# Optimization experiments

Measured on AMD Instinct MI355X. Metric: run time of the kernel, lower is better.

Reference implementation:

```python
import jax, jax.numpy as jnp
import numpy as np

N, IN_C, HID, OUT = 100000, 128, 128, 64
E, EP = 500000, 100000


def _glorot(key, shape):
    fan_in, fan_out = shape[0], shape[1]
    s = jnp.sqrt(6.0 / (fan_in + fan_out))
    return jax.random.uniform(key, shape, jnp.float32, -s, s)


def setup_inputs() -> dict:
    key = jax.random.key(0)
    ks = jax.random.split(key, 10)
    x = jax.random.normal(ks[0], (N, IN_C), jnp.float32)
    edge_index = jax.random.randint(ks[1], (2, E), 0, N, jnp.int64)
    pos_edge_index = jax.random.randint(ks[2], (2, EP), 0, N, jnp.int64)
    neg_edge_index = jax.random.randint(ks[3], (2, EP), 0, N, jnp.int64)
    return {
        "x": x,
        "edge_index": edge_index,
        "pos_edge_index": pos_edge_index,
        "neg_edge_index": neg_edge_index,
        "Wl1": _glorot(ks[4], (IN_C, HID)),
        "Wr1": _glorot(ks[5], (IN_C, HID)),
        "b1": jnp.zeros((HID,), jnp.float32),
        "Wl2": _glorot(ks[6], (HID, OUT)),
        "Wr2": _glorot(ks[7], (HID, OUT)),
        "b2": jnp.zeros((OUT,), jnp.float32),
    }


def sage_conv(x, src, dst, Wl, Wr, b):
    # mean aggregation of neighbor features: messages x[src] scattered to dst
    agg = jax.ops.segment_sum(x[src], dst, num_segments=N)  # (N, D)
    deg = jax.ops.segment_sum(jnp.ones((src.shape[0],), x.dtype), dst, num_segments=N)
    mean = agg / jnp.clip(deg, 1.0, None)[:, None]
    return mean @ Wl + x @ Wr + b


def decode_dot(z, ei):
    return (z[ei[0]] * z[ei[1]]).sum(axis=1)  # (E,)


def reference(x, edge_index, pos_edge_index, neg_edge_index, Wl1, Wr1, b1, Wl2, Wr2, b2):
    src, dst = edge_index[0], edge_index[1]
    h = jax.nn.relu(sage_conv(x, src, dst, Wl1, Wr1, b1))  # dropout off (eval)
    z = sage_conv(h, src, dst, Wl2, Wr2, b2)
    return decode_dot(z, pos_edge_index), decode_dot(z, neg_edge_index)
```

## Files before the change

### kernel.cpp

```cpp
#include <hip/hip_runtime.h>

#define N_NODES 100000
#define NE 500000
#define NEP 100000
#define NBLK_SCAN ((N_NODES + 255) / 256)

typedef short bf16x8 __attribute__((ext_vector_type(8)));
typedef float f32x4  __attribute__((ext_vector_type(4)));
typedef ushort ushort8v __attribute__((ext_vector_type(8)));

__device__ inline ushort f2bf(float f) {
    uint u = __builtin_bit_cast(uint, f);
    return (ushort)((u + 0x7FFFu + ((u >> 16) & 1u)) >> 16);
}
__device__ inline float bf2f(ushort h) {
    uint u = ((uint)h) << 16;
    return __builtin_bit_cast(float, u);
}
__device__ inline float bflo(uint v) { return __builtin_bit_cast(float, v << 16); }
__device__ inline float bfhi(uint v) { return __builtin_bit_cast(float, v & 0xFFFF0000u); }

__global__ __launch_bounds__(256) void hist_kernel(
    const int* __restrict__ ei, int* __restrict__ cnt) {
    int e = blockIdx.x * 256 + threadIdx.x;
    if (e >= NE) return;
    atomicAdd(&cnt[ei[NE + e]], 1);
}

__global__ __launch_bounds__(256) void scan1_kernel(
    const int* __restrict__ cnt, int* __restrict__ off, int* __restrict__ sums) {
    __shared__ int buf[256];
    int t = threadIdx.x;
    int i = blockIdx.x * 256 + t;
    int v = (i < N_NODES) ? cnt[i] : 0;
    buf[t] = v;
    __syncthreads();
#pragma unroll
    for (int d = 1; d < 256; d <<= 1) {
        int add = (t >= d) ? buf[t - d] : 0;
        __syncthreads();
        buf[t] += add;
        __syncthreads();
    }
    if (i < N_NODES) off[i] = buf[t] - v;
    if (t == 255) sums[blockIdx.x] = buf[255];
}

__global__ __launch_bounds__(256) void scan23_kernel(
    int* __restrict__ off, int* __restrict__ off2, const int* __restrict__ sums) {
    __shared__ int red[256];
    int bid = blockIdx.x, t = threadIdx.x;
    int v = 0;
    if (t < bid) v += sums[t];
    if (t + 256 < bid) v += sums[t + 256];
    red[t] = v;
    __syncthreads();
#pragma unroll
    for (int d = 128; d > 0; d >>= 1) {
        if (t < d) red[t] += red[t + d];
        __syncthreads();
    }
    int pre = red[0];
    int i = bid * 256 + t;
    if (i < N_NODES) {
        int o = off[i] + pre;
        off[i] = o;
        off2[i] = o;
    }
    if (i == 0) off[N_NODES] = NE;
}

__global__ __launch_bounds__(256) void fill_kernel(
    const int* __restrict__ ei, int* __restrict__ off2, int* __restrict__ srcS) {
    int e = blockIdx.x * 256 + threadIdx.x;
    if (e >= NE) return;
    int src = ei[e];
    int dst = ei[NE + e];
    int pos = atomicAdd(&off2[dst], 1);
    srcS[pos] = src;
}

__global__ __launch_bounds__(256) void prep_kernel(
    const float* __restrict__ x, ushort* __restrict__ xb,
    const float* __restrict__ Wl1, const float* __restrict__ Wr1,
    ushort* __restrict__ b1h,
    const float* __restrict__ Wl2, const float* __restrict__ Wr2,
    ushort* __restrict__ b2h, int* __restrict__ cnt) {
    int b = blockIdx.x;
    if (b < 6250) {
        size_t i = ((size_t)b * 256 + threadIdx.x) * 8;
        float4 v0 = *reinterpret_cast<const float4*>(x + i);
        float4 v1 = *reinterpret_cast<const float4*>(x + i + 4);
        ushort8v o;
        o[0] = f2bf(v0.x); o[1] = f2bf(v0.y); o[2] = f2bf(v0.z); o[3] = f2bf(v0.w);
        o[4] = f2bf(v1.x); o[5] = f2bf(v1.y); o[6] = f2bf(v1.z); o[7] = f2bf(v1.w);
        *reinterpret_cast<ushort8v*>(xb + i) = o;
    } else if (b < 6250 + 128) {
        int gid = (b - 6250) * 256 + threadIdx.x;
        int r = gid & 7, lane = (gid >> 3) & 63, t = (gid >> 9) & 7, ks = gid >> 12;
        int k = ks * 32 + ((lane >> 4) << 3) + r;
        int n = t * 16 + (lane & 15);
        float v = (k < 128) ? Wl1[k * 128 + n] : Wr1[(k - 128) * 128 + n];
        b1h[gid] = f2bf(v);
    } else if (b < 6442) {
        int gid = (b - 6378) * 256 + threadIdx.x;
        int r = gid & 7, lane = (gid >> 3) & 63, t = (gid >> 9) & 7, ks = gid >> 12;
        int k = ks * 32 + ((lane >> 4) << 3) + r;
        int col = t * 16 + (lane & 15);
        float v = (col < 64) ? Wl2[k * 64 + col] : Wr2[k * 64 + (col - 64)];
        b2h[gid] = f2bf(v);
    } else {
        int i = ((b - 6442) * 256 + threadIdx.x) * 4;
        *reinterpret_cast<int4*>(cnt + i) = make_int4(0, 0, 0, 0);
    }
}

__global__ __launch_bounds__(256) void agg_mean_kernel(
    const ushort* __restrict__ xb, const int* __restrict__ off,
    const int* __restrict__ srcS, ushort* __restrict__ meanH) {
    int n = blockIdx.x * 16 + (threadIdx.x >> 4);
    int l = threadIdx.x & 15;
    int s0 = off[n], s1 = off[n + 1];
    float a0 = 0.f, a1 = 0.f, a2 = 0.f, a3 = 0.f;
    float a4 = 0.f, a5 = 0.f, a6 = 0.f, a7 = 0.f;
    int k = s0;
#define ACCM(v)                                                   \
    { a0 += bflo((v).x); a1 += bfhi((v).x);                       \
      a2 += bflo((v).y); a3 += bfhi((v).y);                       \
      a4 += bflo((v).z); a5 += bfhi((v).z);                       \
      a6 += bflo((v).w); a7 += bfhi((v).w); }
    for (; k + 4 <= s1; k += 4) {
        int sa = srcS[k], sb = srcS[k + 1], sc = srcS[k + 2], sd = srcS[k + 3];
        uint4 va = *(const uint4*)(xb + (size_t)sa * 128 + l * 8);
        uint4 vb = *(const uint4*)(xb + (size_t)sb * 128 + l * 8);
        uint4 vc = *(const uint4*)(xb + (size_t)sc * 128 + l * 8);
        uint4 vd = *(const uint4*)(xb + (size_t)sd * 128 + l * 8);
        ACCM(va) ACCM(vb) ACCM(vc) ACCM(vd)
    }
    for (; k < s1; ++k) {
        uint4 v = *(const uint4*)(xb + (size_t)srcS[k] * 128 + l * 8);
        ACCM(v)
    }
#undef ACCM
    float inv = (s1 > s0) ? 1.0f / (float)(s1 - s0) : 0.0f;
    uint4 o;
    o.x = (uint)f2bf(a0 * inv) | ((uint)f2bf(a1 * inv) << 16);
    o.y = (uint)f2bf(a2 * inv) | ((uint)f2bf(a3 * inv) << 16);
    o.z = (uint)f2bf(a4 * inv) | ((uint)f2bf(a5 * inv) << 16);
    o.w = (uint)f2bf(a6 * inv) | ((uint)f2bf(a7 * inv) << 16);
    *(uint4*)(meanH + (size_t)n * 128 + l * 8) = o;
}

__global__ __launch_bounds__(512) void mlp_kernel(
    const ushort* __restrict__ meanH, const ushort* __restrict__ xb,
    const ushort* __restrict__ b1h, const float* __restrict__ b1,
    const ushort* __restrict__ b2h,
    ushort* __restrict__ tb, ushort* __restrict__ ub) {
    __shared__ __align__(16) ushort Ws[49152];
    __shared__ __align__(16) ushort hs[8][2048];
    const int tid = threadIdx.x;
    const int w = tid >> 6, lane = tid & 63;
    const int lrow = lane & 15, kg = lane >> 4;
    int wid = blockIdx.x * 8 + w;
    if (wid > N_NODES / 16 - 1) wid = N_NODES / 16 - 1;
    const size_t r0 = (size_t)wid * 16;
    char* hw = (char*)&hs[w][0];
    const f32x4 z4 = {0.f, 0.f, 0.f, 0.f};

    bf16x8 aF[8];
#pragma unroll
    for (int ks = 0; ks < 4; ++ks)
        aF[ks] = *(const bf16x8*)(meanH + (r0 + lrow) * 128 + ks * 32 + kg * 8);
#pragma unroll
    for (int ks = 0; ks < 4; ++ks)
        aF[4 + ks] = *(const bf16x8*)(xb + (r0 + lrow) * 128 + ks * 32 + kg * 8);

    {
        const ushort8v* src1 = (const ushort8v*)b1h;
        const ushort8v* src2 = (const ushort8v*)b2h;
        ushort8v* dst = (ushort8v*)Ws;
#pragma unroll
        for (int i = 0; i < 12; ++i) {
            int j = tid + i * 512;
            dst[j] = (j < 4096) ? src1[j] : src2[j - 4096];
        }
    }
    __syncthreads();

    f32x4 acc[8];
#pragma unroll
    for (int t = 0; t < 8; ++t) acc[t] = z4;
#pragma unroll
    for (int ks = 0; ks < 8; ++ks) {
#pragma unroll
        for (int t = 0; t < 8; ++t) {
            bf16x8 Bh = *(const bf16x8*)(Ws + (ks * 8 + t) * 512 + lane * 8);
            acc[t] = __builtin_amdgcn_mfma_f32_16x16x32_bf16(aF[ks], Bh, acc[t], 0, 0, 0);
        }
    }

#pragma unroll
    for (int t = 0; t < 8; ++t) {
        float bj = b1[t * 16 + lrow];
#pragma unroll
        for (int rg = 0; rg < 4; ++rg) {
            int row = kg * 4 + rg;
            int col2 = (t * 16 + lrow) * 2;
            int byte = row * 256 + (col2 ^ ((row & 7) << 4));
            *(ushort*)(hw + byte) = f2bf(fmaxf(acc[t][rg] + bj, 0.0f));
        }
    }

    bf16x8 hF[4];
#pragma unroll
    for (int ks = 0; ks < 4; ++ks) {
        int byte = lrow * 256 + ((ks * 64 + kg * 16) ^ ((lrow & 7) << 4));
        hF[ks] = *(const bf16x8*)(hw + byte);
    }
    f32x4 acc2[8];
#pragma unroll
    for (int t = 0; t < 8; ++t) acc2[t] = z4;
#pragma unroll
    for (int ks = 0; ks < 4; ++ks) {
#pragma unroll
        for (int t = 0; t < 8; ++t) {
            bf16x8 Bh = *(const bf16x8*)(Ws + 32768 + (ks * 8 + t) * 512 + lane * 8);
            acc2[t] = __builtin_amdgcn_mfma_f32_16x16x32_bf16(hF[ks], Bh, acc2[t], 0, 0, 0);
        }
    }

#pragma unroll
    for (int t = 0; t < 8; ++t) {
#pragma unroll
        for (int rg = 0; rg < 4; ++rg) {
            size_t row = r0 + kg * 4 + rg;
            int col = t * 16 + lrow;
            if (t < 4) tb[row * 64 + col] = f2bf(acc2[t][rg]);
            else       ub[row * 64 + (col - 64)] = f2bf(acc2[t][rg]);
        }
    }
}

__global__ __launch_bounds__(256) void agg_z_kernel(
    const ushort* __restrict__ tb, const ushort* __restrict__ ub,
    const float* __restrict__ b2, const int* __restrict__ off,
    const int* __restrict__ srcS, ushort* __restrict__ zb) {
    int n = blockIdx.x * 32 + (threadIdx.x >> 3);
    if (n >= N_NODES) return;
    int l = threadIdx.x & 7;
    int s0 = off[n], s1 = off[n + 1];
    float a0 = 0.f, a1 = 0.f, a2 = 0.f, a3 = 0.f;
    float a4 = 0.f, a5 = 0.f, a6 = 0.f, a7 = 0.f;
    int k = s0;
#define ACCZ(v)                                                   \
    { a0 += bflo((v).x); a1 += bfhi((v).x);                       \
      a2 += bflo((v).y); a3 += bfhi((v).y);                       \
      a4 += bflo((v).z); a5 += bfhi((v).z);                       \
      a6 += bflo((v).w); a7 += bfhi((v).w); }
    for (; k + 4 <= s1; k += 4) {
        int sa = srcS[k], sb = srcS[k + 1], sc = srcS[k + 2], sd = srcS[k + 3];
        uint4 va = *(const uint4*)(tb + (size_t)sa * 64 + l * 8);
        uint4 vb = *(const uint4*)(tb + (size_t)sb * 64 + l * 8);
        uint4 vc = *(const uint4*)(tb + (size_t)sc * 64 + l * 8);
        uint4 vd = *(const uint4*)(tb + (size_t)sd * 64 + l * 8);
        ACCZ(va) ACCZ(vb) ACCZ(vc) ACCZ(vd)
    }
    for (; k < s1; ++k) {
        uint4 v = *(const uint4*)(tb + (size_t)srcS[k] * 64 + l * 8);
        ACCZ(v)
    }
#undef ACCZ
    float inv = (s1 > s0) ? 1.0f / (float)(s1 - s0) : 0.0f;
    uint4 uu = *(const uint4*)(ub + (size_t)n * 64 + l * 8);
    const float* bp = b2 + l * 8;
    uint4 o;
    o.x = (uint)f2bf(a0 * inv + bflo(uu.x) + bp[0]) | ((uint)f2bf(a1 * inv + bfhi(uu.x) + bp[1]) << 16);
    o.y = (uint)f2bf(a2 * inv + bflo(uu.y) + bp[2]) | ((uint)f2bf(a3 * inv + bfhi(uu.y) + bp[3]) << 16);
    o.z = (uint)f2bf(a4 * inv + bflo(uu.z) + bp[4]) | ((uint)f2bf(a5 * inv + bfhi(uu.z) + bp[5]) << 16);
    o.w = (uint)f2bf(a6 * inv + bflo(uu.w) + bp[6]) | ((uint)f2bf(a7 * inv + bfhi(uu.w) + bp[7]) << 16);
    *(uint4*)(zb + (size_t)n * 64 + l * 8) = o;
}

__global__ __launch_bounds__(256) void decode_kernel(
    const ushort* __restrict__ zb,
    const int* __restrict__ pos, const int* __restrict__ neg,
    float* __restrict__ out) {
    int t = blockIdx.x * 256 + threadIdx.x;
    int g = t >> 2;
    int lane = t & 3;
    if (g >= 2 * NEP) return;
    const int* ei;
    int e;
    float* o;
    if (g < NEP) { ei = pos; e = g; o = out; }
    else         { ei = neg; e = g - NEP; o = out + NEP; }
    int a  = ei[e];
    int bn = ei[NEP + e];
    const ushort* ra = zb + (size_t)a  * 64 + lane * 16;
    const ushort* rb = zb + (size_t)bn * 64 + lane * 16;
    uint4 va0 = *reinterpret_cast<const uint4*>(ra);
    uint4 va1 = *reinterpret_cast<const uint4*>(ra + 8);
    uint4 vb0 = *reinterpret_cast<const uint4*>(rb);
    uint4 vb1 = *reinterpret_cast<const uint4*>(rb + 8);
    float s = bflo(va0.x) * bflo(vb0.x) + bfhi(va0.x) * bfhi(vb0.x)
            + bflo(va0.y) * bflo(vb0.y) + bfhi(va0.y) * bfhi(vb0.y)
            + bflo(va0.z) * bflo(vb0.z) + bfhi(va0.z) * bfhi(vb0.z)
            + bflo(va0.w) * bflo(vb0.w) + bfhi(va0.w) * bfhi(vb0.w)
            + bflo(va1.x) * bflo(vb1.x) + bfhi(va1.x) * bfhi(vb1.x)
            + bflo(va1.y) * bflo(vb1.y) + bfhi(va1.y) * bfhi(vb1.y)
            + bflo(va1.z) * bflo(vb1.z) + bfhi(va1.z) * bfhi(vb1.z)
            + bflo(va1.w) * bflo(vb1.w) + bfhi(va1.w) * bfhi(vb1.w);
    s += __shfl_xor(s, 1);
    s += __shfl_xor(s, 2);
    if (lane == 0) o[e] = s;
}

extern "C" void kernel_launch(void* const* d_in, const int* in_sizes, int n_in,
                              void* d_out, int out_size, void* d_ws, size_t ws_size,
                              hipStream_t stream) {
    const float* x    = (const float*)d_in[0];
    const int*   ei   = (const int*)d_in[1];
    const int*   pos  = (const int*)d_in[2];
    const int*   neg  = (const int*)d_in[3];
    const float* Wl1  = (const float*)d_in[4];
    const float* Wr1  = (const float*)d_in[5];
    const float* b1   = (const float*)d_in[6];
    const float* Wl2  = (const float*)d_in[7];
    const float* Wr2  = (const float*)d_in[8];
    const float* b2   = (const float*)d_in[9];
    float* out = (float*)d_out;

    const size_t HALF = (size_t)N_NODES * 128 * 2;
    const size_t QTR  = (size_t)N_NODES * 64 * 2;
    char* ws = (char*)d_ws;
    ushort* xb    = (ushort*)ws;
    ushort* meanH = (ushort*)(ws + HALF);
    ushort* tb    = (ushort*)(ws + 2 * HALF);
    ushort* ub    = (ushort*)(ws + 2 * HALF + QTR);
    ushort* zb    = (ushort*)(ws + 2 * HALF + 2 * QTR);
    int* cnt  = (int*)(ws + 2 * HALF + 3 * QTR);
    int* off  = cnt + N_NODES;
    int* off2 = off + N_NODES + 1;
    int* srcS = off2 + N_NODES;
    int* sums = srcS + NE;
    ushort* b1h = (ushort*)(sums + 512);
    ushort* b2h = b1h + 32768;

    prep_kernel<<<6540, 256, 0, stream>>>(x, xb, Wl1, Wr1, b1h, Wl2, Wr2, b2h, cnt);

    hist_kernel <<<(NE + 255) / 256, 256, 0, stream>>>(ei, cnt);
    scan1_kernel<<<NBLK_SCAN, 256, 0, stream>>>(cnt, off, sums);
    scan23_kernel<<<NBLK_SCAN, 256, 0, stream>>>(off, off2, sums);
    fill_kernel <<<(NE + 255) / 256, 256, 0, stream>>>(ei, off2, srcS);

    agg_mean_kernel<<<N_NODES / 16, 256, 0, stream>>>(xb, off, srcS, meanH);

    mlp_kernel<<<(N_NODES / 16 + 7) / 8, 512, 0, stream>>>(
        meanH, xb, b1h, b1, b2h, tb, ub);

    agg_z_kernel<<<N_NODES / 32 + 1, 256, 0, stream>>>(tb, ub, b2, off, srcS, zb);

    decode_kernel<<<(2 * NEP * 4 + 255) / 256, 256, 0, stream>>>(zb, pos, neg, out);
}
```

Baseline: 141.5 us.

## Spread x-to-bf16 conversion across scan and fill kernels to fill idle CUs

The separate prep kernel that converted x to bf16, packed the weights and zeroed the counts is split up. Zeroing and weight packing now run in a small kernel. The x conversion chunks (2084+2083+2083 = 6250) are appended as extra blocks to the scan1, scan23 and fill kernels, which otherwise launch few blocks. The aim is to hide the bandwidth-bound conversion inside the latency-bound CSR-building kernels and drop one large standalone pass. The cost is heavier launches for those kernels, which may slow the atomic-heavy fill and delay the scan blocks.

Result: no change. 143.1 us (+1.1%).

```diff
diff --git a/kernel.cpp b/kernel.cpp
--- a/kernel.cpp
+++ b/kernel.cpp
@@ -19,6 +19,44 @@
 }
 __device__ inline float bflo(uint v) { return __builtin_bit_cast(float, v << 16); }
 __device__ inline float bfhi(uint v) { return __builtin_bit_cast(float, v & 0xFFFF0000u); }
+
+__device__ inline void convert_chunk(const float* __restrict__ x,
+                                     ushort* __restrict__ xb, int c, int tid) {
+    size_t i = ((size_t)c * 256 + tid) * 8;
+    float4 v0 = *reinterpret_cast<const float4*>(x + i);
+    float4 v1 = *reinterpret_cast<const float4*>(x + i + 4);
+    ushort8v o;
+    o[0] = f2bf(v0.x); o[1] = f2bf(v0.y); o[2] = f2bf(v0.z); o[3] = f2bf(v0.w);
+    o[4] = f2bf(v1.x); o[5] = f2bf(v1.y); o[6] = f2bf(v1.z); o[7] = f2bf(v1.w);
+    *reinterpret_cast<ushort8v*>(xb + i) = o;
+}
+
+__global__ __launch_bounds__(256) void zero_pack_kernel(
+    int* __restrict__ cnt,
+    const float* __restrict__ Wl1, const float* __restrict__ Wr1,
+    ushort* __restrict__ b1h,
+    const float* __restrict__ Wl2, const float* __restrict__ Wr2,
+    ushort* __restrict__ b2h) {
+    int b = blockIdx.x;
+    if (b < 98) {
+        int i = (b * 256 + threadIdx.x) * 4;
+        *reinterpret_cast<int4*>(cnt + i) = make_int4(0, 0, 0, 0);
+    } else if (b < 226) {
+        int gid = (b - 98) * 256 + threadIdx.x;
+        int r = gid & 7, lane = (gid >> 3) & 63, t = (gid >> 9) & 7, ks = gid >> 12;
+        int k = ks * 32 + ((lane >> 4) << 3) + r;
+        int n = t * 16 + (lane & 15);
+        float v = (k < 128) ? Wl1[k * 128 + n] : Wr1[(k - 128) * 128 + n];
+        b1h[gid] = f2bf(v);
+    } else {
+        int gid = (b - 226) * 256 + threadIdx.x;
+        int r = gid & 7, lane = (gid >> 3) & 63, t = (gid >> 9) & 7, ks = gid >> 12;
+        int k = ks * 32 + ((lane >> 4) << 3) + r;
+        int col = t * 16 + (lane & 15);
+        float v = (col < 64) ? Wl2[k * 64 + col] : Wr2[k * 64 + (col - 64)];
+        b2h[gid] = f2bf(v);
+    }
+}
 
 __global__ __launch_bounds__(256) void hist_kernel(
     const int* __restrict__ ei, int* __restrict__ cnt) {
@@ -28,10 +66,15 @@
 }
 
 __global__ __launch_bounds__(256) void scan1_kernel(
-    const int* __restrict__ cnt, int* __restrict__ off, int* __restrict__ sums) {
+    const int* __restrict__ cnt, int* __restrict__ off, int* __restrict__ sums,
+    const float* __restrict__ x, ushort* __restrict__ xb) {
+    int b = blockIdx.x, t = threadIdx.x;
+    if (b >= NBLK_SCAN) {
+        convert_chunk(x, xb, b - NBLK_SCAN, t);
+        return;
+    }
     __shared__ int buf[256];
-    int t = threadIdx.x;
-    int i = blockIdx.x * 256 + t;
+    int i = b * 256 + t;
     int v = (i < N_NODES) ? cnt[i] : 0;
     buf[t] = v;
     __syncthreads();
@@ -43,13 +86,18 @@
         __syncthreads();
     }
     if (i < N_NODES) off[i] = buf[t] - v;
-    if (t == 255) sums[blockIdx.x] = buf[255];
+    if (t == 255) sums[b] = buf[255];
 }
 
 __global__ __launch_bounds__(256) void scan23_kernel(
-    int* __restrict__ off, int* __restrict__ off2, const int* __restrict__ sums) {
+    int* __restrict__ off, int* __restrict__ off2, const int* __restrict__ sums,
+    const float* __restrict__ x, ushort* __restrict__ xb) {
+    int bid = blockIdx.x, t = threadIdx.x;
+    if (bid >= NBLK_SCAN) {
+        convert_chunk(x, xb, 2084 + (bid - NBLK_SCAN), t);
+        return;
+    }
     __shared__ int red[256];
-    int bid = blockIdx.x, t = threadIdx.x;
     int v = 0;
     if (t < bid) v += sums[t];
     if (t + 256 < bid) v += sums[t + 256];
@@ -71,48 +119,20 @@
 }
 
 __global__ __launch_bounds__(256) void fill_kernel(
-    const int* __restrict__ ei, int* __restrict__ off2, int* __restrict__ srcS) {
-    int e = blockIdx.x * 256 + threadIdx.x;
+    const int* __restrict__ ei, int* __restrict__ off2, int* __restrict__ srcS,
+    const float* __restrict__ x, ushort* __restrict__ xb) {
+    int b = blockIdx.x;
+    const int NBF = (NE + 255) / 256;
+    if (b >= NBF) {
+        convert_chunk(x, xb, 4167 + (b - NBF), threadIdx.x);
+        return;
+    }
+    int e = b * 256 + threadIdx.x;
     if (e >= NE) return;
     int src = ei[e];
     int dst = ei[NE + e];
     int pos = atomicAdd(&off2[dst], 1);
     srcS[pos] = src;
-}
-
-__global__ __launch_bounds__(256) void prep_kernel(
-    const float* __restrict__ x, ushort* __restrict__ xb,
-    const float* __restrict__ Wl1, const float* __restrict__ Wr1,
-    ushort* __restrict__ b1h,
-    const float* __restrict__ Wl2, const float* __restrict__ Wr2,
-    ushort* __restrict__ b2h, int* __restrict__ cnt) {
-    int b = blockIdx.x;
-    if (b < 6250) {
-        size_t i = ((size_t)b * 256 + threadIdx.x) * 8;
-        float4 v0 = *reinterpret_cast<const float4*>(x + i);
-        float4 v1 = *reinterpret_cast<const float4*>(x + i + 4);
-        ushort8v o;
-        o[0] = f2bf(v0.x); o[1] = f2bf(v0.y); o[2] = f2bf(v0.z); o[3] = f2bf(v0.w);
-        o[4] = f2bf(v1.x); o[5] = f2bf(v1.y); o[6] = f2bf(v1.z); o[7] = f2bf(v1.w);
-        *reinterpret_cast<ushort8v*>(xb + i) = o;
-    } else if (b < 6250 + 128) {
-        int gid = (b - 6250) * 256 + threadIdx.x;
-        int r = gid & 7, lane = (gid >> 3) & 63, t = (gid >> 9) & 7, ks = gid >> 12;
-        int k = ks * 32 + ((lane >> 4) << 3) + r;
-        int n = t * 16 + (lane & 15);
-        float v = (k < 128) ? Wl1[k * 128 + n] : Wr1[(k - 128) * 128 + n];
-        b1h[gid] = f2bf(v);
-    } else if (b < 6442) {
-        int gid = (b - 6378) * 256 + threadIdx.x;
-        int r = gid & 7, lane = (gid >> 3) & 63, t = (gid >> 9) & 7, ks = gid >> 12;
-        int k = ks * 32 + ((lane >> 4) << 3) + r;
-        int col = t * 16 + (lane & 15);
-        float v = (col < 64) ? Wl2[k * 64 + col] : Wr2[k * 64 + (col - 64)];
-        b2h[gid] = f2bf(v);
-    } else {
-        int i = ((b - 6442) * 256 + threadIdx.x) * 4;
-        *reinterpret_cast<int4*>(cnt + i) = make_int4(0, 0, 0, 0);
-    }
 }
 
 __global__ __launch_bounds__(256) void agg_mean_kernel(
@@ -346,12 +366,14 @@
     ushort* b1h = (ushort*)(sums + 512);
     ushort* b2h = b1h + 32768;
 
-    prep_kernel<<<6540, 256, 0, stream>>>(x, xb, Wl1, Wr1, b1h, Wl2, Wr2, b2h, cnt);
-
-    hist_kernel <<<(NE + 255) / 256, 256, 0, stream>>>(ei, cnt);
-    scan1_kernel<<<NBLK_SCAN, 256, 0, stream>>>(cnt, off, sums);
-    scan23_kernel<<<NBLK_SCAN, 256, 0, stream>>>(off, off2, sums);
-    fill_kernel <<<(NE + 255) / 256, 256, 0, stream>>>(ei, off2, srcS);
+    const int NBF = (NE + 255) / 256;
+
+    zero_pack_kernel<<<290, 256, 0, stream>>>(cnt, Wl1, Wr1, b1h, Wl2, Wr2, b2h);
+
+    hist_kernel  <<<NBF, 256, 0, stream>>>(ei, cnt);
+    scan1_kernel <<<NBLK_SCAN + 2084, 256, 0, stream>>>(cnt, off, sums, x, xb);
+    scan23_kernel<<<NBLK_SCAN + 2083, 256, 0, stream>>>(off, off2, sums, x, xb);
+    fill_kernel  <<<NBF + 2083, 256, 0, stream>>>(ei, off2, srcS, x, xb);
 
     agg_mean_kernel<<<N_NODES / 16, 256, 0, stream>>>(xb, off, srcS, meanH);
 
```
